# Performance work log

Measured on AMD Instinct MI355X. Metric: run time of the kernel, lower is better.

Reference implementation:

```python
import jax, jax.numpy as jnp
from jax import lax
import numpy as np

B, T, I, H, L, C = 64, 512, 128, 256, 2, 3


def _lstm_layer(x, W_ih, W_hh, b_ih, b_hh):
    # x: [B, T, in_dim]; W_ih: [4H, in_dim]; W_hh: [4H, H]
    # PyTorch gate order: i, f, g, o
    gates_x = jnp.einsum('bti,gi->btg', x, W_ih) + b_ih + b_hh  # [B, T, 4H]
    h0 = jnp.zeros((x.shape[0], W_hh.shape[1]), x.dtype)
    c0 = h0

    def step(carry, gx):
        h, c = carry
        g = gx + h @ W_hh.T  # [B, 4H]
        i, f, gg, o = jnp.split(g, 4, axis=-1)
        i = jax.nn.sigmoid(i)
        f = jax.nn.sigmoid(f)
        gg = jnp.tanh(gg)
        o = jax.nn.sigmoid(o)
        c = f * c + i * gg
        h = o * jnp.tanh(c)
        return (h, c), h

    _, hs = lax.scan(step, (h0, c0), jnp.swapaxes(gates_x, 0, 1))  # [T, B, H]
    return jnp.swapaxes(hs, 0, 1)  # [B, T, H]


def setup_inputs() -> dict:
    key = jax.random.key(0)
    ks = jax.random.split(key, 12)
    s = 1.0 / np.sqrt(H)
    u = lambda k, shape: jax.random.uniform(k, shape, jnp.float32, -s, s)
    return {
        'x': jax.random.normal(ks[0], (B, T, I), jnp.float32),
        'W_ih_0': u(ks[1], (4 * H, I)),
        'W_hh_0': u(ks[2], (4 * H, H)),
        'b_ih_0': u(ks[3], (4 * H,)),
        'b_hh_0': u(ks[4], (4 * H,)),
        'W_ih_1': u(ks[5], (4 * H, H)),
        'W_hh_1': u(ks[6], (4 * H, H)),
        'b_ih_1': u(ks[7], (4 * H,)),
        'b_hh_1': u(ks[8], (4 * H,)),
        'fc_w': u(ks[9], (C, H)),
        'fc_b': u(ks[10], (C,)),
    }


def reference(x, W_ih_0, W_hh_0, b_ih_0, b_hh_0, W_ih_1, W_hh_1, b_ih_1, b_hh_1, fc_w, fc_b):
    h = _lstm_layer(x, W_ih_0, W_hh_0, b_ih_0, b_hh_0)
    h = _lstm_layer(h, W_ih_1, W_hh_1, b_ih_1, b_hh_1)
    last = h[:, -1, :]                      # [B, H]
    logits = last @ fc_w.T + fc_b           # [B, C]
    return jax.nn.softmax(logits, axis=1)
```

## Files before the change

### kernel.cpp

```cpp
#include <hip/hip_runtime.h>
#include <cstdint>
#include <cstddef>

typedef _Float16 half2_t __attribute__((ext_vector_type(2)));
typedef _Float16 half8_t __attribute__((ext_vector_type(8)));
typedef float f32x4 __attribute__((ext_vector_type(4)));

static __device__ __forceinline__ float fdot2(half2_t a, half2_t b, float c) {
    return __builtin_amdgcn_fdot2(a, b, c, false);
}
static __device__ __forceinline__ half2_t h2(unsigned int u) {
    return __builtin_bit_cast(half2_t, u);
}
static __device__ __forceinline__ float sigm(float x) {
    return 1.f / (1.f + __expf(-x));
}
static __device__ __forceinline__ float tanh_fast(float x) {
    float ax = fabsf(x);
    float e = __expf(2.f * ax);
    float r = 1.f - 2.f / (e + 1.f);
    return copysignf(r, x);
}

__global__ __launch_bounds__(256) void prep_whh(const float* __restrict__ Whh,
                                                const float* __restrict__ bih,
                                                const float* __restrict__ bhh,
                                                uint4* __restrict__ Wp,
                                                float* __restrict__ bias) {
    int n = blockIdx.x * 256 + threadIdx.x;
    if (n < 1024) bias[n] = bih[n] + bhh[n];
    int p = n >> 9;
    int idx = n & 511;
    int qq = idx >> 8, jj = idx & 255;
    int g = p >> 4, u = p & 15;
    int row = g * 256 + jj;
    int kb = qq * 128 + u * 8;
    union { uint4 u4; _Float16 h[8]; } cv;
#pragma unroll
    for (int i = 0; i < 8; ++i) cv.h[i] = (_Float16)Whh[row * 256 + kb + i];
    Wp[p * 512 + idx] = cv.u4;
}

__global__ __launch_bounds__(256) void cvt_f16(const float* __restrict__ in,
                                               _Float16* __restrict__ out, int n4) {
    int i = blockIdx.x * 256 + threadIdx.x;
    if (i < n4) {
        float4 v = ((const float4*)in)[i];
        union { ushort4 u; _Float16 h[4]; } cv;
        cv.h[0] = (_Float16)v.x; cv.h[1] = (_Float16)v.y;
        cv.h[2] = (_Float16)v.z; cv.h[3] = (_Float16)v.w;
        ((ushort4*)out)[i] = cv.u;
    }
}

__global__ __launch_bounds__(256) void gemm_mfma(const _Float16* __restrict__ A,
                                                 const _Float16* __restrict__ Bw,
                                                 const float* __restrict__ bias,
                                                 float* __restrict__ Cmat, int K) {
    __shared__ _Float16 As[64][72];
    __shared__ _Float16 Bs[64][72];
    const int tid = threadIdx.x;
    const int wave = tid >> 6, lane = tid & 63;
    const int quad = lane >> 4, l16 = lane & 15;
    const int m0 = blockIdx.x * 64, n0 = blockIdx.y * 64;
    const int sr = tid >> 2;
    const int sc = (tid & 3) * 16;

    f32x4 acc[4] = {};

    for (int k0 = 0; k0 < K; k0 += 64) {
        const uint4 a0v = *(const uint4*)(A + (size_t)(m0 + sr) * K + k0 + sc);
        const uint4 a1v = *(const uint4*)(A + (size_t)(m0 + sr) * K + k0 + sc + 8);
        const uint4 b0v = *(const uint4*)(Bw + (size_t)(n0 + sr) * K + k0 + sc);
        const uint4 b1v = *(const uint4*)(Bw + (size_t)(n0 + sr) * K + k0 + sc + 8);
        __syncthreads();
        *(uint4*)&As[sr][sc] = a0v;
        *(uint4*)&As[sr][sc + 8] = a1v;
        *(uint4*)&Bs[sr][sc] = b0v;
        *(uint4*)&Bs[sr][sc + 8] = b1v;
        __syncthreads();
#pragma unroll
        for (int kc = 0; kc < 64; kc += 32) {
            half8_t af = *(const half8_t*)&As[wave * 16 + l16][kc + quad * 8];
#pragma unroll
            for (int nb = 0; nb < 4; ++nb) {
                half8_t bf = *(const half8_t*)&Bs[nb * 16 + l16][kc + quad * 8];
                acc[nb] = __builtin_amdgcn_mfma_f32_16x16x32_f16(af, bf, acc[nb], 0, 0, 0);
            }
        }
    }
#pragma unroll
    for (int nb = 0; nb < 4; ++nb) {
#pragma unroll
        for (int i = 0; i < 4; ++i) {
            int row = m0 + wave * 16 + quad * 4 + i;
            int col = n0 + nb * 16 + l16;
            Cmat[(size_t)row * 1024 + col] = acc[nb][i] + bias[col];
        }
    }
}

__global__ __launch_bounds__(512, 2)
void lstm_scan(const float* __restrict__ gx,
               const uint4* __restrict__ Wp,
               _Float16* __restrict__ h_out,
               int store_all) {
    const int b = blockIdx.x;
    const int tid = threadIdx.x;
    const int q = tid >> 8;
    const int j = tid & 255;

    __shared__ uint4 wlds[16 * 512];
    __shared__ f32x4 pex[512] __attribute__((aligned(16)));
    __shared__ _Float16 hbuf[2][256] __attribute__((aligned(16)));
    __shared__ _Float16 hist[8][256] __attribute__((aligned(16)));

#pragma unroll
    for (int p = 0; p < 16; ++p) wlds[p * 512 + tid] = Wp[(48 + p) * 512 + tid];
    uint4 wreg[48];
#pragma unroll
    for (int p = 0; p < 48; ++p) wreg[p] = Wp[p * 512 + tid];

    if (tid < 256) hbuf[0][tid] = (_Float16)0.f;
    float c = 0.f;
    const float* gxb = gx + (size_t)b * 512 * 1024 + (size_t)(q * 512 + j);
    float gA = gxb[0], gB = gxb[256];
    __syncthreads();

    for (int t = 0; t < 512; ++t) {
        float gA_n = 0.f, gB_n = 0.f;
        if (t < 511) {
            gA_n = gxb[(size_t)(t + 1) * 1024];
            gB_n = gxb[(size_t)(t + 1) * 1024 + 256];
        }

        const char* hpB = (const char*)&hbuf[t & 1][0] + q * 256;

        uint4 hv_p[2], w3_p[2];
        hv_p[0] = *(const uint4*)(hpB + 0 * 16);
        w3_p[0] = wlds[0 * 512 + tid];
        hv_p[1] = *(const uint4*)(hpB + 1 * 16);
        w3_p[1] = wlds[1 * 512 + tid];

        float a0 = 0.f, a1 = 0.f, a2 = 0.f, a3 = 0.f;
#pragma unroll
        for (int u = 0; u < 16; ++u) {
            const uint4 hv = hv_p[u & 1];
            const uint4 w3 = w3_p[u & 1];
            if (u < 14) {
                hv_p[u & 1] = *(const uint4*)(hpB + (u + 2) * 16);
                w3_p[u & 1] = wlds[(u + 2) * 512 + tid];
            }
            const uint4 w0 = wreg[u];
            const uint4 w1 = wreg[16 + u];
            const uint4 w2 = wreg[32 + u];
            a0 = fdot2(h2(w0.x), h2(hv.x), a0);
            a1 = fdot2(h2(w1.x), h2(hv.x), a1);
            a2 = fdot2(h2(w2.x), h2(hv.x), a2);
            a3 = fdot2(h2(w3.x), h2(hv.x), a3);
            a0 = fdot2(h2(w0.y), h2(hv.y), a0);
            a1 = fdot2(h2(w1.y), h2(hv.y), a1);
            a2 = fdot2(h2(w2.y), h2(hv.y), a2);
            a3 = fdot2(h2(w3.y), h2(hv.y), a3);
            a0 = fdot2(h2(w0.z), h2(hv.z), a0);
            a1 = fdot2(h2(w1.z), h2(hv.z), a1);
            a2 = fdot2(h2(w2.z), h2(hv.z), a2);
            a3 = fdot2(h2(w3.z), h2(hv.z), a3);
            a0 = fdot2(h2(w0.w), h2(hv.w), a0);
            a1 = fdot2(h2(w1.w), h2(hv.w), a1);
            a2 = fdot2(h2(w2.w), h2(hv.w), a2);
            a3 = fdot2(h2(w3.w), h2(hv.w), a3);
        }
        if (q == 0) { a0 += gA; a1 += gB; }
        else        { a2 += gA; a3 += gB; }

        f32x4 pv = {a0, a1, a2, a3};
        pex[tid] = pv;
        gA = gA_n; gB = gB_n;
        asm volatile("s_waitcnt lgkmcnt(0)" ::: "memory");
        __builtin_amdgcn_s_barrier();
        asm volatile("" ::: "memory");

        if (tid < 256) {
            const f32x4 v0 = pex[tid];
            const f32x4 v1 = pex[256 + tid];
            const float ai = v0[0] + v1[0];
            const float af = v0[1] + v1[1];
            const float ag = v0[2] + v1[2];
            const float ao = v0[3] + v1[3];
            const float iv = sigm(ai);
            const float fv = sigm(af);
            const float gv = tanh_fast(ag);
            const float ov = sigm(ao);
            c = fv * c + iv * gv;
            const _Float16 hh = (_Float16)(ov * tanh_fast(c));
            hbuf[(t + 1) & 1][tid] = hh;
            if (store_all) hist[t & 7][tid] = hh;
        }
        asm volatile("s_waitcnt lgkmcnt(0)" ::: "memory");
        __builtin_amdgcn_s_barrier();
        asm volatile("" ::: "memory");

        if (store_all && (t & 7) == 7) {
            const uint2 v = ((const uint2*)hist)[tid];
            *(uint2*)(h_out + (size_t)b * 512 * 256 + (size_t)(t - 7) * 256 + tid * 4) = v;
        }
    }
    if (!store_all && tid < 256) {
        h_out[(size_t)b * 256 + tid] = hbuf[0][tid];
    }
}

__global__ __launch_bounds__(64) void fc_softmax(const _Float16* __restrict__ hlast,
                                                 const float* __restrict__ fcw,
                                                 const float* __restrict__ fcb,
                                                 float* __restrict__ out) {
    const int b = blockIdx.x;
    const int lane = threadIdx.x;
    const _Float16* h = hlast + (size_t)b * 256;
    float p0 = 0.f, p1 = 0.f, p2 = 0.f;
    for (int k = lane; k < 256; k += 64) {
        float hv = (float)h[k];
        p0 += hv * fcw[k];
        p1 += hv * fcw[256 + k];
        p2 += hv * fcw[512 + k];
    }
#pragma unroll
    for (int off = 32; off > 0; off >>= 1) {
        p0 += __shfl_down(p0, off);
        p1 += __shfl_down(p1, off);
        p2 += __shfl_down(p2, off);
    }
    if (lane == 0) {
        float l0 = p0 + fcb[0], l1 = p1 + fcb[1], l2 = p2 + fcb[2];
        float m = fmaxf(l0, fmaxf(l1, l2));
        float e0 = __expf(l0 - m), e1 = __expf(l1 - m), e2 = __expf(l2 - m);
        float s = 1.f / (e0 + e1 + e2);
        out[b * 3 + 0] = e0 * s;
        out[b * 3 + 1] = e1 * s;
        out[b * 3 + 2] = e2 * s;
    }
}

extern "C" void kernel_launch(void* const* d_in, const int* in_sizes, int n_in,
                              void* d_out, int out_size, void* d_ws, size_t ws_size,
                              hipStream_t stream) {
    const float* x    = (const float*)d_in[0];
    const float* Wih0 = (const float*)d_in[1];
    const float* Whh0 = (const float*)d_in[2];
    const float* bih0 = (const float*)d_in[3];
    const float* bhh0 = (const float*)d_in[4];
    const float* Wih1 = (const float*)d_in[5];
    const float* Whh1 = (const float*)d_in[6];
    const float* bih1 = (const float*)d_in[7];
    const float* bhh1 = (const float*)d_in[8];
    const float* fcw  = (const float*)d_in[9];
    const float* fcb  = (const float*)d_in[10];
    float* out = (float*)d_out;

    char* ws = (char*)d_ws;
    float* gx        = (float*)ws;     ws += (size_t)32768 * 1024 * 4;
    _Float16* h0f    = (_Float16*)ws;  ws += (size_t)32768 * 256 * 2;
    _Float16* xh     = (_Float16*)ws;  ws += (size_t)32768 * 128 * 2;
    _Float16* hlast  = (_Float16*)ws;  ws += (size_t)64 * 256 * 2;
    _Float16* Wih0h  = (_Float16*)ws;  ws += (size_t)1024 * 128 * 2;
    _Float16* Wih1h  = (_Float16*)ws;  ws += (size_t)1024 * 256 * 2;
    uint4* Wp0       = (uint4*)ws;     ws += (size_t)1024 * 256 * 2;
    uint4* Wp1       = (uint4*)ws;     ws += (size_t)1024 * 256 * 2;
    float* bias0     = (float*)ws;     ws += 4096;
    float* bias1     = (float*)ws;     ws += 4096;

    prep_whh<<<128, 256, 0, stream>>>(Whh0, bih0, bhh0, Wp0, bias0);
    prep_whh<<<128, 256, 0, stream>>>(Whh1, bih1, bhh1, Wp1, bias1);
    cvt_f16<<<4096, 256, 0, stream>>>(x, xh, 32768 * 128 / 4);
    cvt_f16<<<128, 256, 0, stream>>>(Wih0, Wih0h, 1024 * 128 / 4);
    cvt_f16<<<256, 256, 0, stream>>>(Wih1, Wih1h, 1024 * 256 / 4);

    gemm_mfma<<<dim3(512, 16), 256, 0, stream>>>(xh, Wih0h, bias0, gx, 128);
    lstm_scan<<<64, 512, 0, stream>>>(gx, Wp0, h0f, 1);

    gemm_mfma<<<dim3(512, 16), 256, 0, stream>>>(h0f, Wih1h, bias1, gx, 256);
    lstm_scan<<<64, 512, 0, stream>>>(gx, Wp1, hlast, 0);

    fc_softmax<<<64, 64, 0, stream>>>(hlast, fcw, fcb, out);
}
```

Measured before the change: 1.635 ms.

## Repartition LSTM recurrent matvec to four K-quarters with broadcast h loads

Reorganizes the packed W_hh layout and the lstm_scan thread mapping so each wave handles one quarter of the hidden K dimension and 128 output rows across 8 gate slices, instead of a half-K split over 4 gates. Each h vector load is now uniform within a wave (LDS broadcast) and reused across 8 accumulators, which cuts per-thread LDS traffic for h. The trade-off is a 4-way partial-sum reduction through shared memory with selects, replacing the previous 2-way one.

```diff
diff --git a/kernel.cpp b/kernel.cpp
--- a/kernel.cpp
+++ b/kernel.cpp
@@ -20,6 +20,13 @@
     float e = __expf(2.f * ax);
     float r = 1.f - 2.f / (e + 1.f);
     return copysignf(r, x);
+}
+static __device__ __forceinline__ float dot4(const uint4 w, const uint4 h, float a) {
+    a = fdot2(h2(w.x), h2(h.x), a);
+    a = fdot2(h2(w.y), h2(h.y), a);
+    a = fdot2(h2(w.z), h2(h.z), a);
+    a = fdot2(h2(w.w), h2(h.w), a);
+    return a;
 }
 
 __global__ __launch_bounds__(256) void prep_whh(const float* __restrict__ Whh,
@@ -30,15 +37,15 @@
     int n = blockIdx.x * 256 + threadIdx.x;
     if (n < 1024) bias[n] = bih[n] + bhh[n];
     int p = n >> 9;
-    int idx = n & 511;
-    int qq = idx >> 8, jj = idx & 255;
-    int g = p >> 4, u = p & 15;
-    int row = g * 256 + jj;
-    int kb = qq * 128 + u * 8;
+    int e = n & 511;
+    int m = p >> 3, cc = p & 7;
+    int kq = e >> 7, sl = e & 127;
+    int row = sl + 128 * m;
+    int kb = kq * 64 + cc * 8;
     union { uint4 u4; _Float16 h[8]; } cv;
 #pragma unroll
     for (int i = 0; i < 8; ++i) cv.h[i] = (_Float16)Whh[row * 256 + kb + i];
-    Wp[p * 512 + idx] = cv.u4;
+    Wp[p * 512 + e] = cv.u4;
 }
 
 __global__ __launch_bounds__(256) void cvt_f16(const float* __restrict__ in,
@@ -105,97 +112,100 @@
                const uint4* __restrict__ Wp,
                _Float16* __restrict__ h_out,
                int store_all) {
+    const int tid = threadIdx.x;
     const int b = blockIdx.x;
-    const int tid = threadIdx.x;
-    const int q = tid >> 8;
-    const int j = tid & 255;
+    const int w = tid >> 6, l = tid & 63;
+    const int kq = w & 3;
+    const int s = w >> 2;
+    const int sl = s * 64 + l;
+    const int e = kq * 128 + sl;
 
     __shared__ uint4 wlds[16 * 512];
-    __shared__ f32x4 pex[512] __attribute__((aligned(16)));
+    __shared__ float pex[4 * 2 * 128 * 4] __attribute__((aligned(16)));
     __shared__ _Float16 hbuf[2][256] __attribute__((aligned(16)));
     __shared__ _Float16 hist[8][256] __attribute__((aligned(16)));
 
 #pragma unroll
-    for (int p = 0; p < 16; ++p) wlds[p * 512 + tid] = Wp[(48 + p) * 512 + tid];
+    for (int p = 0; p < 16; ++p) wlds[p * 512 + tid] = Wp[(48 + p) * 512 + e];
     uint4 wreg[48];
 #pragma unroll
-    for (int p = 0; p < 48; ++p) wreg[p] = Wp[p * 512 + tid];
+    for (int p = 0; p < 48; ++p) wreg[p] = Wp[p * 512 + e];
 
     if (tid < 256) hbuf[0][tid] = (_Float16)0.f;
     float c = 0.f;
-    const float* gxb = gx + (size_t)b * 512 * 1024 + (size_t)(q * 512 + j);
-    float gA = gxb[0], gB = gxb[256];
+    const float* gxb = gx + (size_t)b * 512 * 1024;
+    float gA = gxb[e], gB = gxb[e + 512];
     __syncthreads();
+
+    f32x4* pexv = (f32x4*)pex;
+    const int jh = (tid & 255) >> 7;
+    const int js = tid & 127;
 
     for (int t = 0; t < 512; ++t) {
         float gA_n = 0.f, gB_n = 0.f;
         if (t < 511) {
-            gA_n = gxb[(size_t)(t + 1) * 1024];
-            gB_n = gxb[(size_t)(t + 1) * 1024 + 256];
-        }
-
-        const char* hpB = (const char*)&hbuf[t & 1][0] + q * 256;
-
-        uint4 hv_p[2], w3_p[2];
-        hv_p[0] = *(const uint4*)(hpB + 0 * 16);
-        w3_p[0] = wlds[0 * 512 + tid];
-        hv_p[1] = *(const uint4*)(hpB + 1 * 16);
-        w3_p[1] = wlds[1 * 512 + tid];
+            gA_n = gxb[(size_t)(t + 1) * 1024 + e];
+            gB_n = gxb[(size_t)(t + 1) * 1024 + e + 512];
+        }
+
+        const uint4* hb = (const uint4*)&hbuf[t & 1][0] + kq * 8;
+
+        uint4 wsP = wlds[0 * 512 + tid];
+        uint4 wsQ = wlds[8 * 512 + tid];
 
         float a0 = 0.f, a1 = 0.f, a2 = 0.f, a3 = 0.f;
-#pragma unroll
-        for (int u = 0; u < 16; ++u) {
-            const uint4 hv = hv_p[u & 1];
-            const uint4 w3 = w3_p[u & 1];
-            if (u < 14) {
-                hv_p[u & 1] = *(const uint4*)(hpB + (u + 2) * 16);
-                w3_p[u & 1] = wlds[(u + 2) * 512 + tid];
+        float a4 = 0.f, a5 = 0.f, a6 = 0.f, a7 = 0.f;
+#pragma unroll
+        for (int cc = 0; cc < 8; ++cc) {
+            const uint4 hv = hb[cc];
+            const uint4 w6 = wsP, w7 = wsQ;
+            if (cc < 7) {
+                wsP = wlds[(cc + 1) * 512 + tid];
+                wsQ = wlds[(9 + cc) * 512 + tid];
             }
-            const uint4 w0 = wreg[u];
-            const uint4 w1 = wreg[16 + u];
-            const uint4 w2 = wreg[32 + u];
-            a0 = fdot2(h2(w0.x), h2(hv.x), a0);
-            a1 = fdot2(h2(w1.x), h2(hv.x), a1);
-            a2 = fdot2(h2(w2.x), h2(hv.x), a2);
-            a3 = fdot2(h2(w3.x), h2(hv.x), a3);
-            a0 = fdot2(h2(w0.y), h2(hv.y), a0);
-            a1 = fdot2(h2(w1.y), h2(hv.y), a1);
-            a2 = fdot2(h2(w2.y), h2(hv.y), a2);
-            a3 = fdot2(h2(w3.y), h2(hv.y), a3);
-            a0 = fdot2(h2(w0.z), h2(hv.z), a0);
-            a1 = fdot2(h2(w1.z), h2(hv.z), a1);
-            a2 = fdot2(h2(w2.z), h2(hv.z), a2);
-            a3 = fdot2(h2(w3.z), h2(hv.z), a3);
-            a0 = fdot2(h2(w0.w), h2(hv.w), a0);
-            a1 = fdot2(h2(w1.w), h2(hv.w), a1);
-            a2 = fdot2(h2(w2.w), h2(hv.w), a2);
-            a3 = fdot2(h2(w3.w), h2(hv.w), a3);
-        }
-        if (q == 0) { a0 += gA; a1 += gB; }
-        else        { a2 += gA; a3 += gB; }
-
-        f32x4 pv = {a0, a1, a2, a3};
-        pex[tid] = pv;
+            a0 = dot4(wreg[cc],      hv, a0);
+            a1 = dot4(wreg[8 + cc],  hv, a1);
+            a2 = dot4(wreg[16 + cc], hv, a2);
+            a3 = dot4(wreg[24 + cc], hv, a3);
+            a4 = dot4(wreg[32 + cc], hv, a4);
+            a5 = dot4(wreg[40 + cc], hv, a5);
+            a6 = dot4(w6, hv, a6);
+            a7 = dot4(w7, hv, a7);
+        }
+        if (kq == 0)      { a0 += gA; a4 += gB; }
+        else if (kq == 1) { a1 += gA; a5 += gB; }
+        else if (kq == 2) { a2 += gA; a6 += gB; }
+        else              { a3 += gA; a7 += gB; }
+
+        f32x4 lo = {a0, a1, a2, a3};
+        f32x4 hi = {a4, a5, a6, a7};
+        pexv[(kq * 2 + 0) * 128 + sl] = lo;
+        pexv[(kq * 2 + 1) * 128 + sl] = hi;
         gA = gA_n; gB = gB_n;
         asm volatile("s_waitcnt lgkmcnt(0)" ::: "memory");
         __builtin_amdgcn_s_barrier();
         asm volatile("" ::: "memory");
 
         if (tid < 256) {
-            const f32x4 v0 = pex[tid];
-            const f32x4 v1 = pex[256 + tid];
-            const float ai = v0[0] + v1[0];
-            const float af = v0[1] + v1[1];
-            const float ag = v0[2] + v1[2];
-            const float ao = v0[3] + v1[3];
-            const float iv = sigm(ai);
-            const float fv = sigm(af);
-            const float gv = tanh_fast(ag);
-            const float ov = sigm(ao);
+            const int j = tid;
+            float Ai = 0.f, Af = 0.f, Ag = 0.f, Ao = 0.f;
+#pragma unroll
+            for (int k2 = 0; k2 < 4; ++k2) {
+                const f32x4 v0 = pexv[(k2 * 2 + 0) * 128 + js];
+                const f32x4 v1 = pexv[(k2 * 2 + 1) * 128 + js];
+                Ai += jh ? v0[1] : v0[0];
+                Af += jh ? v0[3] : v0[2];
+                Ag += jh ? v1[1] : v1[0];
+                Ao += jh ? v1[3] : v1[2];
+            }
+            const float iv = sigm(Ai);
+            const float fv = sigm(Af);
+            const float gv = tanh_fast(Ag);
+            const float ov = sigm(Ao);
             c = fv * c + iv * gv;
             const _Float16 hh = (_Float16)(ov * tanh_fast(c));
-            hbuf[(t + 1) & 1][tid] = hh;
-            if (store_all) hist[t & 7][tid] = hh;
+            hbuf[(t + 1) & 1][j] = hh;
+            if (store_all) hist[t & 7][j] = hh;
         }
         asm volatile("s_waitcnt lgkmcnt(0)" ::: "memory");
         __builtin_amdgcn_s_barrier();
```

Result: slower. 1.953 ms (+19.5%).
